# Performance work log

Measured on AMD Instinct MI355X. Metric: run time of the kernel, lower is better.

The kernel has to match this reference:

```python
import jax, jax.numpy as jnp
import numpy as np

B, L, H, E, D = 4, 2048, 8, 64, 64  # seq S == L (causal mask requires square scores)


def setup_inputs() -> dict:
    key = jax.random.key(0)
    k0, k1, k2, k3, k4 = jax.random.split(key, 5)
    queries = jax.random.normal(k0, (B, L, H, E), jnp.float32)
    keys = jax.random.normal(k1, (B, L, H, E), jnp.float32)
    values = jax.random.normal(k2, (B, L, H, D), jnp.float32)
    # per-sample learned de-stationary scale (positive) and bias
    tau = jax.random.uniform(k3, (B, 1, 1), jnp.float32, 0.5, 1.5)
    delta = jax.random.normal(k4, (B, 1, L), jnp.float32) * 0.1
    return {"queries": queries, "keys": keys, "values": values, "tau": tau, "delta": delta}


def reference(queries, keys, values, tau, delta):
    Bq, Lq, Hq, Eq = queries.shape
    S = keys.shape[1]
    scale = 1.0 / jnp.sqrt(jnp.asarray(Eq, jnp.float32))
    # torch path: rearrange('b s h d l -> (b d) s h l') with s=h=d=1 -> [B,1,1,1] / [B,1,1,S]
    tau_b = tau.reshape(Bq, 1, 1, 1)
    delta_b = delta.reshape(Bq, 1, 1, -1)[..., :S]
    # scores: [B, H, L, S]
    scores = jnp.einsum('blhe,bshe->bhls', queries, keys) * tau_b + delta_b
    causal = jnp.triu(jnp.ones((Lq, S), bool), k=1)  # True above diagonal -> masked
    scores = jnp.where(causal, -jnp.inf, scores)
    A = jax.nn.softmax(scale * scores, axis=-1)  # dropout is identity in eval/reference
    V = jnp.einsum('bhls,bshd->blhd', A, values)  # [B, L, H, D]
    return V
```

## Files before the change

### kernel.cpp

```cpp
#include <hip/hip_runtime.h>
#include <hip/hip_bf16.h>

#define Bsz 4
#define Lsz 2048
#define Hsz 8

typedef __attribute__((ext_vector_type(8)))  short bf16x8;
typedef __attribute__((ext_vector_type(4)))  float f32x4;
typedef __attribute__((ext_vector_type(16))) float f32x16;
typedef __attribute__((ext_vector_type(2)))  unsigned u32x2;

__device__ __forceinline__ short f2bs(float f) {
    union { float f; unsigned u; } v; v.f = f;
    unsigned r = v.u + 0x7FFFu + ((v.u >> 16) & 1u);
    return (short)(r >> 16);
}
__device__ __forceinline__ unsigned cvtpk(float lo, float hi) {
    unsigned r;
    asm("v_cvt_pk_bf16_f32 %0, %1, %2" : "=v"(r) : "v"(lo), "v"(hi));
    return r;
}

__device__ __forceinline__ void stage16(const short* g, short* l) {
    __builtin_amdgcn_global_load_lds(
        (const __attribute__((address_space(1))) unsigned int*)g,
        (__attribute__((address_space(3))) unsigned int*)l,
        16, 0, 0);
}

__global__ __launch_bounds__(256) void prep_kv(
    const float* __restrict__ ksrc, const float* __restrict__ vsrc,
    short* __restrict__ Kf, short* __restrict__ Vf)
{
    __shared__ float Tl[64][65];
    const int raw = blockIdx.x;
    const int tid = threadIdx.x;
    const bool isK = raw < Bsz*Hsz*32;
    const int bid = isK ? raw : raw - Bsz*Hsz*32;
    const int tl = bid & 31, bh = bid >> 5;
    const int b = bh >> 3, h = bh & 7;

    const int row = tid >> 2, c0 = (tid & 3) * 16;
    const float* src = (isK ? ksrc : vsrc)
                     + (((size_t)b*Lsz + tl*64 + row)*Hsz + h)*64 + c0;
    *(float4*)&Tl[row][c0]      = *(const float4*)(src);
    *(float4*)&Tl[row][c0 + 4]  = *(const float4*)(src + 4);
    *(float4*)&Tl[row][c0 + 8]  = *(const float4*)(src + 8);
    *(float4*)&Tl[row][c0 + 12] = *(const float4*)(src + 12);
    __syncthreads();

    const int lane = tid & 63, l31 = lane & 31, hi = lane >> 5;
    if (isK) {
        short* dst = Kf + (size_t)bid * 4096;
        #pragma unroll
        for (int cc = 0; cc < 2; ++cc) {
            const int c  = (tid >> 6)*2 + cc;
            const int kh = c >> 2, eb = c & 3;
            const float* rp = &Tl[kh*32 + l31][eb*16 + hi*8];
            bf16x8 o = {f2bs(rp[0]),f2bs(rp[1]),f2bs(rp[2]),f2bs(rp[3]),
                        f2bs(rp[4]),f2bs(rp[5]),f2bs(rp[6]),f2bs(rp[7])};
            *(bf16x8*)(dst + c*512 + lane*8) = o;
        }
    } else {
        short* dst = Vf + (size_t)bid * 4096;
        #pragma unroll
        for (int cc = 0; cc < 2; ++cc) {
            const int c  = (tid >> 6)*2 + cc;
            const int dh = c >> 2, kb = c & 3;
            const int d  = dh*32 + l31;
            const int s0 = kb*16 + hi*8;
            bf16x8 o = {f2bs(Tl[s0+0][d]), f2bs(Tl[s0+1][d]),
                        f2bs(Tl[s0+2][d]), f2bs(Tl[s0+3][d]),
                        f2bs(Tl[s0+4][d]), f2bs(Tl[s0+5][d]),
                        f2bs(Tl[s0+6][d]), f2bs(Tl[s0+7][d])};
            *(bf16x8*)(dst + c*512 + lane*8) = o;
        }
    }
}

__global__ __launch_bounds__(256, 4) void dsattn_main(
    const float* __restrict__ q,
    const short* __restrict__ Kf,
    const short* __restrict__ Vf,
    const float* __restrict__ tau,
    const float* __restrict__ delta,
    float* __restrict__ out)
{
    __shared__ __align__(16) short Kb[2][4096];
    __shared__ __align__(16) short Vb[2][4096];
    __shared__ float dls[Lsz];

    const int tid  = threadIdx.x;
    const int wv   = tid >> 6;
    const int lane = tid & 63;
    const int l31  = lane & 31;
    const int hi   = lane >> 5;
    const int qh   = wv & 1;
    const int kh   = wv >> 1;

    const int bh = blockIdx.x;
    const int b  = bh >> 3, h = bh & 7;
    const int j  = blockIdx.y, aj = j & 7, gj = j >> 3;
    const int qt = (gj == 0) ? 31 - 2*aj : (gj == 1) ? 30 - 2*aj
                 : (gj == 2) ? 2*aj + 1  : 2*aj;
    const int q0 = qt * 64;
    const int T  = qt + 1;

    const float c2  = 0.125f * 1.44269504f;
    const float st2 = c2 * tau[b];

    const short* kt = Kf + (size_t)bh * (32*4096);
    const short* vt = Vf + (size_t)bh * (32*4096);

    const short* gsrc = ((wv < 2) ? kt : vt) + (wv & 1)*2048 + lane*8;

#define STAGE(buf) do {                                                     \
        short* lb_ = (wv < 2 ? &Kb[(buf)][0] : &Vb[(buf)][0]) + (wv&1)*2048;\
        stage16(gsrc + 0*512, lb_ + 0*512);                                 \
        stage16(gsrc + 1*512, lb_ + 1*512);                                 \
        stage16(gsrc + 2*512, lb_ + 2*512);                                 \
        stage16(gsrc + 3*512, lb_ + 3*512);                                 \
        gsrc += 4096;                                                       \
    } while (0)

    STAGE(0);

    {
        const float* dsrc = delta + (size_t)b*Lsz + tid*8;
        float4 a = *(const float4*)(dsrc);
        float4 c = *(const float4*)(dsrc + 4);
        a.x*=c2; a.y*=c2; a.z*=c2; a.w*=c2;
        c.x*=c2; c.y*=c2; c.z*=c2; c.w*=c2;
        *(float4*)&dls[tid*8]     = a;
        *(float4*)&dls[tid*8 + 4] = c;
    }

    bf16x8 qf[4];
    {
        const float* qrow = q + (((size_t)b*Lsz + q0 + qh*32 + l31)*Hsz + h)*64 + hi*8;
        #pragma unroll
        for (int eb = 0; eb < 4; ++eb) {
            float4 a0 = *(const float4*)(qrow + eb*16);
            float4 a1 = *(const float4*)(qrow + eb*16 + 4);
            qf[eb] = (bf16x8){f2bs(a0.x),f2bs(a0.y),f2bs(a0.z),f2bs(a0.w),
                              f2bs(a1.x),f2bs(a1.y),f2bs(a1.z),f2bs(a1.w)};
        }
    }

    f32x16 oacc0, oacc1;
    #pragma unroll
    for (int i = 0; i < 16; ++i) { oacc0[i] = 0.f; oacc1[i] = 0.f; }
    float l_acc = 0.f;

    __syncthreads();

#define TILE_BODY(t_, MASKED) do {                                          \
        const int cur_ = (t_) & 1;                                          \
        const short* Kc_ = &Kb[cur_][0];                                    \
        const short* Vc_ = &Vb[cur_][0];                                    \
        const int k0_ = (t_)*64;                                            \
         \
        f32x16 sacc;                                                        \
        _Pragma("unroll")                                                   \
        for (int i = 0; i < 16; ++i) sacc[i] = 0.f;                         \
        __builtin_amdgcn_s_setprio(1);                                      \
        _Pragma("unroll")                                                   \
        for (int eb = 0; eb < 4; ++eb) {                                    \
            bf16x8 kf_ = *(const bf16x8*)(Kc_ + (kh*4 + eb)*512 + lane*8);  \
            sacc = __builtin_amdgcn_mfma_f32_32x32x16_bf16(kf_, qf[eb], sacc, 0,0,0); \
        }                                                                   \
        __builtin_amdgcn_s_setprio(0);                                      \
        if (MASKED) {                                                       \
            const int qrw_ = qh*32 + l31;                                   \
            _Pragma("unroll")                                               \
            for (int g = 0; g < 4; ++g)                                     \
                _Pragma("unroll")                                           \
                for (int i = 0; i < 4; ++i)                                 \
                    if (kh*32 + 8*g + 4*hi + i > qrw_) sacc[g*4+i] = -1e30f;\
        }                                                                   \
                                           \
        float p_[16];                                                       \
        _Pragma("unroll")                                                   \
        for (int g = 0; g < 4; ++g) {                                       \
            f32x4 dlv_ = *(const f32x4*)&dls[k0_ + kh*32 + g*8 + hi*4];     \
            _Pragma("unroll")                                               \
            for (int i = 0; i < 4; ++i)                                     \
                p_[g*4+i] = __builtin_amdgcn_exp2f(fmaf(sacc[g*4+i], st2, dlv_[i])); \
            l_acc += (p_[g*4]+p_[g*4+1]) + (p_[g*4+2]+p_[g*4+3]);           \
        }                                                                   \
                \
        bf16x8 pf_[2];                                                      \
        _Pragma("unroll")                                                   \
        for (int kb = 0; kb < 2; ++kb) {                                    \
            unsigned a0_ = cvtpk(p_[kb*8+0], p_[kb*8+1]);                   \
            unsigned a1_ = cvtpk(p_[kb*8+2], p_[kb*8+3]);                   \
            unsigned b0_ = cvtpk(p_[kb*8+4], p_[kb*8+5]);                   \
            unsigned b1_ = cvtpk(p_[kb*8+6], p_[kb*8+7]);                   \
            u32x2 s0_ = __builtin_amdgcn_permlane32_swap(a0_, b0_, false, false); \
            u32x2 s1_ = __builtin_amdgcn_permlane32_swap(a1_, b1_, false, false); \
            union { unsigned u[4]; bf16x8 v; } pk_;                         \
            pk_.u[0] = s0_[0]; pk_.u[1] = s1_[0];                           \
            pk_.u[2] = s0_[1]; pk_.u[3] = s1_[1];                           \
            pf_[kb] = pk_.v;                                                \
        }                                                                   \
                               \
        __builtin_amdgcn_s_setprio(1);                                      \
        _Pragma("unroll")                                                   \
        for (int kb = 0; kb < 2; ++kb) {                                    \
            bf16x8 vf0_ = *(const bf16x8*)(Vc_ + (     kh*2 + kb)*512 + lane*8); \
            bf16x8 vf1_ = *(const bf16x8*)(Vc_ + (4 +  kh*2 + kb)*512 + lane*8); \
            oacc0 = __builtin_amdgcn_mfma_f32_32x32x16_bf16(vf0_, pf_[kb], oacc0, 0,0,0); \
            oacc1 = __builtin_amdgcn_mfma_f32_32x32x16_bf16(vf1_, pf_[kb], oacc1, 0,0,0); \
        }                                                                   \
        __builtin_amdgcn_s_setprio(0);                                      \
    } while (0)

    for (int t = 0; t + 1 < T; ++t) {
        STAGE((t + 1) & 1);
        TILE_BODY(t, false);
        __syncthreads();
    }
    TILE_BODY(T - 1, true);

    float lw = l_acc + __shfl_xor(l_acc, 32, 64);
    float* Ored = (float*)&Kb[0][0];
    float* lred = (float*)&Vb[0][0];
    __syncthreads();

    if (kh == 1) {
        #pragma unroll
        for (int g = 0; g < 4; ++g)
            #pragma unroll
            for (int i = 0; i < 4; ++i) {
                const int d_ = 8*g + 4*hi + i;
                Ored[(qh*64 +      d_)*32 + l31] = oacc0[g*4+i];
                Ored[(qh*64 + 32 + d_)*32 + l31] = oacc1[g*4+i];
            }
        if (lane < 32) lred[qh*32 + l31] = lw;
    }
    __syncthreads();

    if (kh == 0) {
        const float invl = 1.0f / (lw + lred[qh*32 + l31]);
        float* orow = out + (((size_t)b*Lsz + q0 + qh*32 + l31)*Hsz + h)*64;
        #pragma unroll
        for (int g = 0; g < 4; ++g) {
            const int d_ = 8*g + 4*hi;
            float4 o0, o1;
            o0.x = (oacc0[g*4+0] + Ored[(qh*64 + d_ + 0)*32 + l31]) * invl;
            o0.y = (oacc0[g*4+1] + Ored[(qh*64 + d_ + 1)*32 + l31]) * invl;
            o0.z = (oacc0[g*4+2] + Ored[(qh*64 + d_ + 2)*32 + l31]) * invl;
            o0.w = (oacc0[g*4+3] + Ored[(qh*64 + d_ + 3)*32 + l31]) * invl;
            o1.x = (oacc1[g*4+0] + Ored[(qh*64 + 32 + d_ + 0)*32 + l31]) * invl;
            o1.y = (oacc1[g*4+1] + Ored[(qh*64 + 32 + d_ + 1)*32 + l31]) * invl;
            o1.z = (oacc1[g*4+2] + Ored[(qh*64 + 32 + d_ + 2)*32 + l31]) * invl;
            o1.w = (oacc1[g*4+3] + Ored[(qh*64 + 32 + d_ + 3)*32 + l31]) * invl;
            *(float4*)(orow + d_)      = o0;
            *(float4*)(orow + 32 + d_) = o1;
        }
    }
#undef STAGE
#undef TILE_BODY
}

extern "C" void kernel_launch(void* const* d_in, const int* in_sizes, int n_in,
                              void* d_out, int out_size, void* d_ws, size_t ws_size,
                              hipStream_t stream) {
    (void)in_sizes; (void)n_in; (void)out_size; (void)ws_size;
    const float* q     = (const float*)d_in[0];
    const float* k     = (const float*)d_in[1];
    const float* v     = (const float*)d_in[2];
    const float* tau   = (const float*)d_in[3];
    const float* delta = (const float*)d_in[4];
    float* out = (float*)d_out;

    short* Kf = (short*)d_ws;
    short* Vf = (short*)d_ws + (size_t)(4*1024*1024);

    prep_kv<<<dim3(Bsz*Hsz*32*2), dim3(256), 0, stream>>>(k, v, Kf, Vf);
    dsattn_main<<<dim3(Bsz*Hsz, 32), dim3(256), 0, stream>>>(q, Kf, Vf, tau, delta, out);
}
```

Measured before the change: 123.9 us.

## Give each wave private K/V buffers and drop per-tile block barriers

Shrinks the block from four waves to two. Each wave now covers both 32-row query halves for its own 32-key slice and stages its own K and V chunks into a private double buffer. Per-tile __syncthreads is replaced by explicit vmcnt waits, so waves no longer block on each other. The V layout in prep_kv is permuted so each wave's V chunk is contiguous, and the tile scheduling order is reshuffled. This raises per-wave register pressure (four output accumulators) and halves threads per block, which risks lower occupancy and less latency hiding.

Result: slower. 133.8 us (+8.0%).

```diff
diff --git a/kernel.cpp b/kernel.cpp
--- a/kernel.cpp
+++ b/kernel.cpp
@@ -67,18 +67,19 @@
         for (int cc = 0; cc < 2; ++cc) {
             const int c  = (tid >> 6)*2 + cc;
             const int dh = c >> 2, kb = c & 3;
+            const int cp = (kb >> 1)*4 + dh*2 + (kb & 1);
             const int d  = dh*32 + l31;
             const int s0 = kb*16 + hi*8;
             bf16x8 o = {f2bs(Tl[s0+0][d]), f2bs(Tl[s0+1][d]),
                         f2bs(Tl[s0+2][d]), f2bs(Tl[s0+3][d]),
                         f2bs(Tl[s0+4][d]), f2bs(Tl[s0+5][d]),
                         f2bs(Tl[s0+6][d]), f2bs(Tl[s0+7][d])};
-            *(bf16x8*)(dst + c*512 + lane*8) = o;
-        }
-    }
-}
-
-__global__ __launch_bounds__(256, 4) void dsattn_main(
+            *(bf16x8*)(dst + cp*512 + lane*8) = o;
+        }
+    }
+}
+
+__global__ __launch_bounds__(128, 2) void dsattn_main(
     const float* __restrict__ q,
     const short* __restrict__ Kf,
     const short* __restrict__ Vf,
@@ -86,180 +87,207 @@
     const float* __restrict__ delta,
     float* __restrict__ out)
 {
-    __shared__ __align__(16) short Kb[2][4096];
-    __shared__ __align__(16) short Vb[2][4096];
+    __shared__ __align__(16) short Wb[2][2][4096];
     __shared__ float dls[Lsz];
 
     const int tid  = threadIdx.x;
-    const int wv   = tid >> 6;
+    const int kh   = tid >> 6;
     const int lane = tid & 63;
     const int l31  = lane & 31;
     const int hi   = lane >> 5;
-    const int qh   = wv & 1;
-    const int kh   = wv >> 1;
 
     const int bh = blockIdx.x;
     const int b  = bh >> 3, h = bh & 7;
-    const int j  = blockIdx.y, aj = j & 7, gj = j >> 3;
-    const int qt = (gj == 0) ? 31 - 2*aj : (gj == 1) ? 30 - 2*aj
-                 : (gj == 2) ? 2*aj + 1  : 2*aj;
+    const int y = blockIdx.y, g8 = y >> 3, a = y & 7;
+    const int qt = (g8 == 0) ? 31 - 2*a : (g8 == 1) ? 2*a
+                 : (g8 == 2) ? 30 - 2*a : 2*a + 1;
     const int q0 = qt * 64;
     const int T  = qt + 1;
 
     const float c2  = 0.125f * 1.44269504f;
     const float st2 = c2 * tau[b];
 
-    const short* kt = Kf + (size_t)bh * (32*4096);
-    const short* vt = Vf + (size_t)bh * (32*4096);
-
-    const short* gsrc = ((wv < 2) ? kt : vt) + (wv & 1)*2048 + lane*8;
+    const short* gK = Kf + (size_t)bh*(32*4096) + kh*2048 + lane*8;
+    const short* gV = Vf + (size_t)bh*(32*4096) + kh*2048 + lane*8;
+    short* const myb = &Wb[kh][0][0];
 
 #define STAGE(buf) do {                                                     \
-        short* lb_ = (wv < 2 ? &Kb[(buf)][0] : &Vb[(buf)][0]) + (wv&1)*2048;\
-        stage16(gsrc + 0*512, lb_ + 0*512);                                 \
-        stage16(gsrc + 1*512, lb_ + 1*512);                                 \
-        stage16(gsrc + 2*512, lb_ + 2*512);                                 \
-        stage16(gsrc + 3*512, lb_ + 3*512);                                 \
-        gsrc += 4096;                                                       \
+        short* lb_ = myb + (buf)*4096;                                      \
+        stage16(gK + 0*512, lb_ + 0*512);                                   \
+        stage16(gK + 1*512, lb_ + 1*512);                                   \
+        stage16(gK + 2*512, lb_ + 2*512);                                   \
+        stage16(gK + 3*512, lb_ + 3*512);                                   \
+        stage16(gV + 0*512, lb_ + 2048 + 0*512);                            \
+        stage16(gV + 1*512, lb_ + 2048 + 1*512);                            \
+        stage16(gV + 2*512, lb_ + 2048 + 2*512);                            \
+        stage16(gV + 3*512, lb_ + 2048 + 3*512);                            \
+        gK += 4096; gV += 4096;                                             \
+        __builtin_amdgcn_sched_barrier(0);                                  \
     } while (0)
 
+#define WAITN(n) do {                                                       \
+        asm volatile("s_waitcnt vmcnt(" #n ")" ::: "memory");               \
+        __builtin_amdgcn_sched_barrier(0);                                  \
+    } while (0)
+
     STAGE(0);
 
     {
-        const float* dsrc = delta + (size_t)b*Lsz + tid*8;
-        float4 a = *(const float4*)(dsrc);
-        float4 c = *(const float4*)(dsrc + 4);
-        a.x*=c2; a.y*=c2; a.z*=c2; a.w*=c2;
-        c.x*=c2; c.y*=c2; c.z*=c2; c.w*=c2;
-        *(float4*)&dls[tid*8]     = a;
-        *(float4*)&dls[tid*8 + 4] = c;
-    }
-
-    bf16x8 qf[4];
-    {
+        const float* dsrc = delta + (size_t)b*Lsz + tid*16;
+        #pragma unroll
+        for (int u = 0; u < 4; ++u) {
+            float4 v = *(const float4*)(dsrc + u*4);
+            v.x*=c2; v.y*=c2; v.z*=c2; v.w*=c2;
+            *(float4*)&dls[tid*16 + u*4] = v;
+        }
+    }
+
+    bf16x8 qf[4][2];
+    #pragma unroll
+    for (int qh = 0; qh < 2; ++qh) {
         const float* qrow = q + (((size_t)b*Lsz + q0 + qh*32 + l31)*Hsz + h)*64 + hi*8;
         #pragma unroll
         for (int eb = 0; eb < 4; ++eb) {
             float4 a0 = *(const float4*)(qrow + eb*16);
             float4 a1 = *(const float4*)(qrow + eb*16 + 4);
-            qf[eb] = (bf16x8){f2bs(a0.x),f2bs(a0.y),f2bs(a0.z),f2bs(a0.w),
-                              f2bs(a1.x),f2bs(a1.y),f2bs(a1.z),f2bs(a1.w)};
-        }
-    }
-
-    f32x16 oacc0, oacc1;
+            qf[eb][qh] = (bf16x8){f2bs(a0.x),f2bs(a0.y),f2bs(a0.z),f2bs(a0.w),
+                                  f2bs(a1.x),f2bs(a1.y),f2bs(a1.z),f2bs(a1.w)};
+        }
+    }
+
+    f32x16 oacc[2][2];
     #pragma unroll
-    for (int i = 0; i < 16; ++i) { oacc0[i] = 0.f; oacc1[i] = 0.f; }
-    float l_acc = 0.f;
+    for (int dh = 0; dh < 2; ++dh)
+        #pragma unroll
+        for (int qh = 0; qh < 2; ++qh)
+            #pragma unroll
+            for (int i = 0; i < 16; ++i) oacc[dh][qh][i] = 0.f;
+    float l_a0 = 0.f, l_a1 = 0.f;
 
     __syncthreads();
 
-#define TILE_BODY(t_, MASKED) do {                                          \
-        const int cur_ = (t_) & 1;                                          \
-        const short* Kc_ = &Kb[cur_][0];                                    \
-        const short* Vc_ = &Vb[cur_][0];                                    \
+#define TILE_BODY(t_, MASKED, HASNEXT) do {                                 \
+        const short* cb_ = myb + ((t_) & 1)*4096;                           \
         const int k0_ = (t_)*64;                                            \
-         \
-        f32x16 sacc;                                                        \
-        _Pragma("unroll")                                                   \
-        for (int i = 0; i < 16; ++i) sacc[i] = 0.f;                         \
+        if (HASNEXT) STAGE(((t_)+1) & 1);                                   \
+        if (HASNEXT) WAITN(12); else WAITN(4);           \
+        f32x16 s0_, s1_;                                                    \
+        _Pragma("unroll")                                                   \
+        for (int i = 0; i < 16; ++i) { s0_[i] = 0.f; s1_[i] = 0.f; }        \
         __builtin_amdgcn_s_setprio(1);                                      \
         _Pragma("unroll")                                                   \
         for (int eb = 0; eb < 4; ++eb) {                                    \
-            bf16x8 kf_ = *(const bf16x8*)(Kc_ + (kh*4 + eb)*512 + lane*8);  \
-            sacc = __builtin_amdgcn_mfma_f32_32x32x16_bf16(kf_, qf[eb], sacc, 0,0,0); \
+            bf16x8 kf_ = *(const bf16x8*)(cb_ + eb*512 + lane*8);           \
+            s0_ = __builtin_amdgcn_mfma_f32_32x32x16_bf16(kf_, qf[eb][0], s0_, 0,0,0); \
+            s1_ = __builtin_amdgcn_mfma_f32_32x32x16_bf16(kf_, qf[eb][1], s1_, 0,0,0); \
         }                                                                   \
         __builtin_amdgcn_s_setprio(0);                                      \
         if (MASKED) {                                                       \
-            const int qrw_ = qh*32 + l31;                                   \
             _Pragma("unroll")                                               \
             for (int g = 0; g < 4; ++g)                                     \
                 _Pragma("unroll")                                           \
-                for (int i = 0; i < 4; ++i)                                 \
-                    if (kh*32 + 8*g + 4*hi + i > qrw_) sacc[g*4+i] = -1e30f;\
+                for (int i = 0; i < 4; ++i) {                               \
+                    const int ky_ = kh*32 + 8*g + 4*hi + i;                 \
+                    if (ky_ >      l31) s0_[g*4+i] = -1e30f;                \
+                    if (ky_ > 32 + l31) s1_[g*4+i] = -1e30f;                \
+                }                                                           \
         }                                                                   \
-                                           \
-        float p_[16];                                                       \
+        float p0_[16], p1_[16];                                             \
         _Pragma("unroll")                                                   \
         for (int g = 0; g < 4; ++g) {                                       \
             f32x4 dlv_ = *(const f32x4*)&dls[k0_ + kh*32 + g*8 + hi*4];     \
             _Pragma("unroll")                                               \
-            for (int i = 0; i < 4; ++i)                                     \
-                p_[g*4+i] = __builtin_amdgcn_exp2f(fmaf(sacc[g*4+i], st2, dlv_[i])); \
-            l_acc += (p_[g*4]+p_[g*4+1]) + (p_[g*4+2]+p_[g*4+3]);           \
+            for (int i = 0; i < 4; ++i) {                                   \
+                p0_[g*4+i] = __builtin_amdgcn_exp2f(fmaf(s0_[g*4+i], st2, dlv_[i])); \
+                p1_[g*4+i] = __builtin_amdgcn_exp2f(fmaf(s1_[g*4+i], st2, dlv_[i])); \
+            }                                                               \
+            l_a0 += (p0_[g*4]+p0_[g*4+1]) + (p0_[g*4+2]+p0_[g*4+3]);        \
+            l_a1 += (p1_[g*4]+p1_[g*4+1]) + (p1_[g*4+2]+p1_[g*4+3]);        \
         }                                                                   \
-                \
-        bf16x8 pf_[2];                                                      \
+        bf16x8 pf0_[2], pf1_[2];                                            \
         _Pragma("unroll")                                                   \
         for (int kb = 0; kb < 2; ++kb) {                                    \
-            unsigned a0_ = cvtpk(p_[kb*8+0], p_[kb*8+1]);                   \
-            unsigned a1_ = cvtpk(p_[kb*8+2], p_[kb*8+3]);                   \
-            unsigned b0_ = cvtpk(p_[kb*8+4], p_[kb*8+5]);                   \
-            unsigned b1_ = cvtpk(p_[kb*8+6], p_[kb*8+7]);                   \
-            u32x2 s0_ = __builtin_amdgcn_permlane32_swap(a0_, b0_, false, false); \
-            u32x2 s1_ = __builtin_amdgcn_permlane32_swap(a1_, b1_, false, false); \
+            unsigned a0_ = cvtpk(p0_[kb*8+0], p0_[kb*8+1]);                 \
+            unsigned a1_ = cvtpk(p0_[kb*8+2], p0_[kb*8+3]);                 \
+            unsigned b0_ = cvtpk(p0_[kb*8+4], p0_[kb*8+5]);                 \
+            unsigned b1_ = cvtpk(p0_[kb*8+6], p0_[kb*8+7]);                 \
+            u32x2 s0s_ = __builtin_amdgcn_permlane32_swap(a0_, b0_, false, false); \
+            u32x2 s1s_ = __builtin_amdgcn_permlane32_swap(a1_, b1_, false, false); \
             union { unsigned u[4]; bf16x8 v; } pk_;                         \
-            pk_.u[0] = s0_[0]; pk_.u[1] = s1_[0];                           \
-            pk_.u[2] = s0_[1]; pk_.u[3] = s1_[1];                           \
-            pf_[kb] = pk_.v;                                                \
+            pk_.u[0] = s0s_[0]; pk_.u[1] = s1s_[0];                         \
+            pk_.u[2] = s0s_[1]; pk_.u[3] = s1s_[1];                         \
+            pf0_[kb] = pk_.v;                                               \
+            unsigned c0_ = cvtpk(p1_[kb*8+0], p1_[kb*8+1]);                 \
+            unsigned c1_ = cvtpk(p1_[kb*8+2], p1_[kb*8+3]);                 \
+            unsigned d0_ = cvtpk(p1_[kb*8+4], p1_[kb*8+5]);                 \
+            unsigned d1_ = cvtpk(p1_[kb*8+6], p1_[kb*8+7]);                 \
+            u32x2 s2s_ = __builtin_amdgcn_permlane32_swap(c0_, d0_, false, false); \
+            u32x2 s3s_ = __builtin_amdgcn_permlane32_swap(c1_, d1_, false, false); \
+            union { unsigned u[4]; bf16x8 v; } pk2_;                        \
+            pk2_.u[0] = s2s_[0]; pk2_.u[1] = s3s_[0];                       \
+            pk2_.u[2] = s2s_[1]; pk2_.u[3] = s3s_[1];                       \
+            pf1_[kb] = pk2_.v;                                              \
         }                                                                   \
-                               \
+        if (HASNEXT) WAITN(8); else WAITN(0);            \
         __builtin_amdgcn_s_setprio(1);                                      \
         _Pragma("unroll")                                                   \
-        for (int kb = 0; kb < 2; ++kb) {                                    \
-            bf16x8 vf0_ = *(const bf16x8*)(Vc_ + (     kh*2 + kb)*512 + lane*8); \
-            bf16x8 vf1_ = *(const bf16x8*)(Vc_ + (4 +  kh*2 + kb)*512 + lane*8); \
-            oacc0 = __builtin_amdgcn_mfma_f32_32x32x16_bf16(vf0_, pf_[kb], oacc0, 0,0,0); \
-            oacc1 = __builtin_amdgcn_mfma_f32_32x32x16_bf16(vf1_, pf_[kb], oacc1, 0,0,0); \
-        }                                                                   \
+        for (int kb = 0; kb < 2; ++kb)                                      \
+            _Pragma("unroll")                                               \
+            for (int dh = 0; dh < 2; ++dh) {                                \
+                bf16x8 vf_ = *(const bf16x8*)(cb_ + 2048 + (dh*2+kb)*512 + lane*8); \
+                oacc[dh][0] = __builtin_amdgcn_mfma_f32_32x32x16_bf16(vf_, pf0_[kb], oacc[dh][0], 0,0,0); \
+                oacc[dh][1] = __builtin_amdgcn_mfma_f32_32x32x16_bf16(vf_, pf1_[kb], oacc[dh][1], 0,0,0); \
+            }                                                               \
         __builtin_amdgcn_s_setprio(0);                                      \
     } while (0)
 
-    for (int t = 0; t + 1 < T; ++t) {
-        STAGE((t + 1) & 1);
-        TILE_BODY(t, false);
-        __syncthreads();
-    }
-    TILE_BODY(T - 1, true);
-
-    float lw = l_acc + __shfl_xor(l_acc, 32, 64);
-    float* Ored = (float*)&Kb[0][0];
-    float* lred = (float*)&Vb[0][0];
+    for (int t = 0; t < T - 1; ++t) TILE_BODY(t, false, true);
+    TILE_BODY(T - 1, true, false);
+
+    float lw0 = l_a0 + __shfl_xor(l_a0, 32, 64);
+    float lw1 = l_a1 + __shfl_xor(l_a1, 32, 64);
+    float* Ored = (float*)&Wb[0][0][0];
+    float* lred = Ored + 4096;
     __syncthreads();
 
     if (kh == 1) {
         #pragma unroll
-        for (int g = 0; g < 4; ++g)
+        for (int qh = 0; qh < 2; ++qh)
             #pragma unroll
-            for (int i = 0; i < 4; ++i) {
-                const int d_ = 8*g + 4*hi + i;
-                Ored[(qh*64 +      d_)*32 + l31] = oacc0[g*4+i];
-                Ored[(qh*64 + 32 + d_)*32 + l31] = oacc1[g*4+i];
-            }
-        if (lane < 32) lred[qh*32 + l31] = lw;
+            for (int dh = 0; dh < 2; ++dh)
+                #pragma unroll
+                for (int g = 0; g < 4; ++g)
+                    #pragma unroll
+                    for (int i = 0; i < 4; ++i) {
+                        const int d_ = dh*32 + 8*g + 4*hi + i;
+                        Ored[(qh*64 + d_)*32 + l31] = oacc[dh][qh][g*4+i];
+                    }
+        if (lane < 32) { lred[l31] = lw0; lred[32 + l31] = lw1; }
     }
     __syncthreads();
 
     if (kh == 0) {
-        const float invl = 1.0f / (lw + lred[qh*32 + l31]);
-        float* orow = out + (((size_t)b*Lsz + q0 + qh*32 + l31)*Hsz + h)*64;
-        #pragma unroll
-        for (int g = 0; g < 4; ++g) {
-            const int d_ = 8*g + 4*hi;
-            float4 o0, o1;
-            o0.x = (oacc0[g*4+0] + Ored[(qh*64 + d_ + 0)*32 + l31]) * invl;
-            o0.y = (oacc0[g*4+1] + Ored[(qh*64 + d_ + 1)*32 + l31]) * invl;
-            o0.z = (oacc0[g*4+2] + Ored[(qh*64 + d_ + 2)*32 + l31]) * invl;
-            o0.w = (oacc0[g*4+3] + Ored[(qh*64 + d_ + 3)*32 + l31]) * invl;
-            o1.x = (oacc1[g*4+0] + Ored[(qh*64 + 32 + d_ + 0)*32 + l31]) * invl;
-            o1.y = (oacc1[g*4+1] + Ored[(qh*64 + 32 + d_ + 1)*32 + l31]) * invl;
-            o1.z = (oacc1[g*4+2] + Ored[(qh*64 + 32 + d_ + 2)*32 + l31]) * invl;
-            o1.w = (oacc1[g*4+3] + Ored[(qh*64 + 32 + d_ + 3)*32 + l31]) * invl;
-            *(float4*)(orow + d_)      = o0;
-            *(float4*)(orow + 32 + d_) = o1;
+        #pragma unroll
+        for (int qh = 0; qh < 2; ++qh) {
+            const float lw = (qh == 0) ? lw0 : lw1;
+            const float invl = 1.0f / (lw + lred[qh*32 + l31]);
+            float* orow = out + (((size_t)b*Lsz + q0 + qh*32 + l31)*Hsz + h)*64;
+            #pragma unroll
+            for (int dh = 0; dh < 2; ++dh)
+                #pragma unroll
+                for (int g = 0; g < 4; ++g) {
+                    const int d_ = dh*32 + 8*g + 4*hi;
+                    float4 o;
+                    o.x = (oacc[dh][qh][g*4+0] + Ored[(qh*64 + d_ + 0)*32 + l31]) * invl;
+                    o.y = (oacc[dh][qh][g*4+1] + Ored[(qh*64 + d_ + 1)*32 + l31]) * invl;
+                    o.z = (oacc[dh][qh][g*4+2] + Ored[(qh*64 + d_ + 2)*32 + l31]) * invl;
+                    o.w = (oacc[dh][qh][g*4+3] + Ored[(qh*64 + d_ + 3)*32 + l31]) * invl;
+                    *(float4*)(orow + d_) = o;
+                }
         }
     }
 #undef STAGE
+#undef WAITN
 #undef TILE_BODY
 }
 
@@ -278,5 +306,5 @@
     short* Vf = (short*)d_ws + (size_t)(4*1024*1024);
 
     prep_kv<<<dim3(Bsz*Hsz*32*2), dim3(256), 0, stream>>>(k, v, Kf, Vf);
-    dsattn_main<<<dim3(Bsz*Hsz, 32), dim3(256), 0, stream>>>(q, Kf, Vf, tau, delta, out);
-}
+    dsattn_main<<<dim3(Bsz*Hsz, 32), dim3(128), 0, stream>>>(q, Kf, Vf, tau, delta, out);
+}
```
